# Kernel optimization log

Hardware: AMD Instinct MI355X
Metric: run time of the kernel (lower is better)

Reference implementation:

```python
import jax, jax.numpy as jnp
import numpy as np

N = 4096
IN_F = 512
OUT_F = 256
HEADS = 4
HEAD_DIM = OUT_F // HEADS


def setup_inputs() -> dict:
    key = jax.random.key(0)
    k_feat, k_adj, k_w, k_a = jax.random.split(key, 4)
    features = jax.random.normal(k_feat, (N, IN_F), dtype=jnp.float32)
    adj_matrix = jax.random.uniform(k_adj, (N, N), dtype=jnp.float32)
    # xavier-uniform-ish init scaled small
    W = jax.random.normal(k_w, (OUT_F, IN_F), dtype=jnp.float32) * (1.0 / np.sqrt(IN_F))
    a = jax.random.normal(k_a, (HEADS, 2 * HEAD_DIM), dtype=jnp.float32) * 0.1
    bias = jnp.zeros((OUT_F,), dtype=jnp.float32)
    return {"features": features, "adj_matrix": adj_matrix, "W": W, "a": a, "bias": bias}


def reference(features, adj_matrix, W, a, bias):
    n = features.shape[0]
    h = features @ W.T                      # [N, OUT_F]
    hh = h.reshape(n, HEADS, HEAD_DIM)      # [N, H, D]
    # e[i,j,h] = leaky_relu(<h_i, a[:, :D]> + <h_j, a[:, D:]>) -- additive decomposition
    e_src = jnp.einsum('nhd,hd->nh', hh, a[:, :HEAD_DIM])   # [N, H]
    e_dst = jnp.einsum('nhd,hd->nh', hh, a[:, HEAD_DIM:])   # [N, H]
    e = e_src[:, None, :] + e_dst[None, :, :]               # [N, N, H]
    e = jnp.where(e >= 0, e, 0.2 * e)                       # leaky_relu(0.2)
    mask = adj_matrix[:, :, None] > 0.1                     # [N, N, 1]
    e = jnp.where(mask, e, -jnp.inf)
    attention = jax.nn.softmax(e, axis=1)                   # softmax over j
    attention = jnp.nan_to_num(attention, nan=0.0)          # fully-masked rows -> 0
    attention_mean = attention.mean(axis=2)                 # [N, N]
    h_out = attention_mean @ h + bias                       # [N, OUT_F]
    return h_out
```

## Files before the change

### kernel.cpp

```cpp
#include <hip/hip_runtime.h>
#include <math.h>

#define NN      4096
#define INF_    512
#define OUTF    256
#define NHEAD   4
#define HDIM    64
#define KSPLIT  8

typedef __attribute__((ext_vector_type(8))) short  short8x;
typedef __attribute__((ext_vector_type(4))) float  float4x;
typedef __attribute__((ext_vector_type(2))) float  float2x;

__device__ __forceinline__ unsigned short f2bf(float x) {
    union { float f; unsigned int u; } c; c.f = x;
    unsigned int r = (c.u + 0x7FFFu + ((c.u >> 16) & 1u)) >> 16;
    return (unsigned short)r;
}
__device__ __forceinline__ unsigned int cvtpk_bf16(float lo, float hi) {
    unsigned int r;
    asm("v_cvt_pk_bf16_f32 %0, %1, %2" : "=v"(r) : "v"(lo), "v"(hi));
    return r;
}
__device__ __forceinline__ float2x bf2up(unsigned int u) {
    union { unsigned int x; float f; } lo, hi;
    lo.x = u << 16; hi.x = u & 0xFFFF0000u;
    float2x r; r[0] = lo.f; r[1] = hi.f; return r;
}
__device__ __forceinline__ float2x max2(float2x a, float2x b) {
    float2x r; r[0] = fmaxf(a[0], b[0]); r[1] = fmaxf(a[1], b[1]); return r;
}

__global__ __launch_bounds__(256) void k_cast(const float* __restrict__ feat,
                                              const float* __restrict__ W,
                                              const float* __restrict__ bias,
                                              unsigned short* __restrict__ featb,
                                              unsigned short* __restrict__ Wb,
                                              float* __restrict__ out) {
    const int b = blockIdx.x;
    const int tid = threadIdx.x;
    if (b >= 2176) {
        int idx = (b - 2176) * 1024 + tid * 4;
        float4x bv = *(const float4x*)(bias + ((tid * 4) & 255));
        *(float4x*)(out + idx) = bv;
        return;
    }
    const float* src;
    unsigned short* dst;
    int idx;
    if (b < 2048) { src = feat; dst = featb; idx = b * 1024 + tid * 4; }
    else          { src = W;    dst = Wb;    idx = (b - 2048) * 1024 + tid * 4; }
    float4x v = *(const float4x*)(src + idx);
    ushort4 u;
    u.x = f2bf(v[0]); u.y = f2bf(v[1]); u.z = f2bf(v[2]); u.w = f2bf(v[3]);
    *(ushort4*)(dst + idx) = u;
}

__global__ __launch_bounds__(256) void k_hedge(const unsigned short* __restrict__ featb,
                                               const unsigned short* __restrict__ Wb,
                                               const float* __restrict__ a,
                                               unsigned short* __restrict__ hT,
                                               float* __restrict__ es,
                                               unsigned short* __restrict__ Bt,
                                               unsigned short* __restrict__ Dt) {
    __shared__ __align__(16) unsigned short lds_f[32 * 40];
    __shared__ __align__(16) unsigned short lds_w[256 * 40];
    const int tid  = threadIdx.x;
    const int w    = tid >> 6;
    const int lane = tid & 63;
    const int lidx = lane & 15;
    const int quad = lane >> 4;
    const int i0   = blockIdx.x * 32;
    const int srf  = tid >> 3;
    const int skf  = (tid & 7) * 4;
    const int srw  = tid >> 2;
    const int skw  = (tid & 3) * 8;

    float4x acc[2][4];
    #pragma unroll
    for (int p = 0; p < 2; ++p)
        #pragma unroll
        for (int q = 0; q < 4; ++q)
            acc[p][q] = (float4x){0.f, 0.f, 0.f, 0.f};

    for (int kt = 0; kt < INF_; kt += 32) {
        __syncthreads();
        *(ushort4*)&lds_f[srf * 40 + skf] = *(const ushort4*)&featb[(size_t)(i0 + srf) * INF_ + kt + skf];
        #pragma unroll
        for (int itr = 0; itr < 4; ++itr) {
            int n = itr * 64 + srw;
            *(ushort4*)&lds_w[n * 40 + skw]     = *(const ushort4*)&Wb[(size_t)n * INF_ + kt + skw];
            *(ushort4*)&lds_w[n * 40 + skw + 4] = *(const ushort4*)&Wb[(size_t)n * INF_ + kt + skw + 4];
        }
        __syncthreads();
        short8x af[2], bw[4];
        #pragma unroll
        for (int t = 0; t < 2; ++t)
            af[t] = *(const short8x*)&lds_f[(t * 16 + lidx) * 40 + quad * 8];
        #pragma unroll
        for (int t = 0; t < 4; ++t)
            bw[t] = *(const short8x*)&lds_w[(w * 64 + t * 16 + lidx) * 40 + quad * 8];
        #pragma unroll
        for (int it = 0; it < 2; ++it)
            #pragma unroll
            for (int nt = 0; nt < 4; ++nt)
                acc[it][nt] = __builtin_amdgcn_mfma_f32_16x16x32_bf16(
                    af[it], bw[nt], acc[it][nt], 0, 0, 0);
    }
    #pragma unroll
    for (int it = 0; it < 2; ++it)
        #pragma unroll
        for (int nt = 0; nt < 4; ++nt) {
            int col = w * 64 + nt * 16 + lidx;
            int m0r = i0 + it * 16 + quad * 4;
            uint2 u;
            u.x = cvtpk_bf16(acc[it][nt][0], acc[it][nt][1]);
            u.y = cvtpk_bf16(acc[it][nt][2], acc[it][nt][3]);
            *(uint2*)&hT[(size_t)col * NN + m0r] = u;
        }
    float asrc[4], adst[4];
    #pragma unroll
    for (int nt = 0; nt < 4; ++nt) {
        asrc[nt] = a[w * 2 * HDIM + nt * 16 + lidx];
        adst[nt] = a[w * 2 * HDIM + HDIM + nt * 16 + lidx];
    }
    #pragma unroll
    for (int it = 0; it < 2; ++it)
        #pragma unroll
        for (int r = 0; r < 4; ++r) {
            float s = 0.f, d = 0.f;
            #pragma unroll
            for (int nt = 0; nt < 4; ++nt) {
                s += acc[it][nt][r] * asrc[nt];
                d += acc[it][nt][r] * adst[nt];
            }
            #pragma unroll
            for (int off = 1; off < 16; off <<= 1) {
                s += __shfl_xor(s, off);
                d += __shfl_xor(d, off);
            }
            if (lidx == 0) {
                int row = i0 + it * 16 + quad * 4 + r;
                es[row * NHEAD + w] = s;
                Bt[row * NHEAD + w] = f2bf(__expf(d));
                Dt[row * NHEAD + w] = f2bf(__expf(0.2f * d));
            }
        }
}

__global__ __launch_bounds__(256) void k_attn(const float* __restrict__ adj,
                                              const float* __restrict__ es,
                                              const unsigned short* __restrict__ Bt,
                                              const unsigned short* __restrict__ Dt,
                                              unsigned short* __restrict__ attn) {
    __shared__ float red[4][4];
    __shared__ float cfs[4];
    const int tid = threadIdx.x;
    const int wv  = tid >> 6;
    const int lane = tid & 63;
    const int i = blockIdx.x;

    const float4x esv = ((const float4x*)es)[i];
    float2x A01, A23, C01, C23;
    A01[0] = __expf(esv[0]); A01[1] = __expf(esv[1]);
    A23[0] = __expf(esv[2]); A23[1] = __expf(esv[3]);
    C01[0] = __expf(0.2f * esv[0]); C01[1] = __expf(0.2f * esv[1]);
    C23[0] = __expf(0.2f * esv[2]); C23[1] = __expf(0.2f * esv[3]);

    const float4x* arow4 = (const float4x*)(adj + (size_t)i * NN);
    const uint4* B4 = (const uint4*)Bt;
    const uint4* D4 = (const uint4*)Dt;

    float2x m01[4][4], m23[4][4];
    float2x den01 = (float2x){0.f, 0.f};
    float2x den23 = (float2x){0.f, 0.f};
    #pragma unroll
    for (int t = 0; t < 4; ++t) {
        int jv = t * 256 + tid;
        float4x av = arow4[jv];
        uint4 bu0 = B4[jv * 2], bu1 = B4[jv * 2 + 1];
        uint4 du0 = D4[jv * 2], du1 = D4[jv * 2 + 1];
        unsigned int bwv[8] = {bu0.x, bu0.y, bu0.z, bu0.w, bu1.x, bu1.y, bu1.z, bu1.w};
        unsigned int dwv[8] = {du0.x, du0.y, du0.z, du0.w, du1.x, du1.y, du1.z, du1.w};
        #pragma unroll
        for (int u = 0; u < 4; ++u) {
            float2x b01 = bf2up(bwv[u * 2]);
            float2x b23 = bf2up(bwv[u * 2 + 1]);
            float2x d01 = bf2up(dwv[u * 2]);
            float2x d23 = bf2up(dwv[u * 2 + 1]);
            float mf = (av[u] > 0.1f) ? 1.f : 0.f;
            float2x mf2; mf2[0] = mf; mf2[1] = mf;
            m01[t][u] = mf2 * max2(A01 * b01, C01 * d01);
            m23[t][u] = mf2 * max2(A23 * b23, C23 * d23);
            den01 += m01[t][u];
            den23 += m23[t][u];
        }
    }
    float dh[4] = {den01[0], den01[1], den23[0], den23[1]};
    #pragma unroll
    for (int off = 1; off < 64; off <<= 1) {
        #pragma unroll
        for (int h = 0; h < 4; ++h)
            dh[h] += __shfl_xor(dh[h], off);
    }
    if (lane == 0) {
        #pragma unroll
        for (int h = 0; h < 4; ++h) red[wv][h] = dh[h];
    }
    __syncthreads();
    if (tid < 4)
        cfs[tid] = red[0][tid] + red[1][tid] + red[2][tid] + red[3][tid];
    __syncthreads();
    float sc[4];
    #pragma unroll
    for (int h = 0; h < 4; ++h) {
        float den = cfs[h];
        sc[h] = den > 0.f ? 0.25f / den : 0.f;
    }

    unsigned short* orow = attn + (size_t)i * NN;
    #pragma unroll
    for (int t = 0; t < 4; ++t) {
        int jv = t * 256 + tid;
        float pv[4];
        #pragma unroll
        for (int u = 0; u < 4; ++u) {
            pv[u] = sc[0] * m01[t][u][0] + sc[1] * m01[t][u][1]
                  + sc[2] * m23[t][u][0] + sc[3] * m23[t][u][1];
        }
        uint2 o;
        o.x = cvtpk_bf16(pv[0], pv[1]);
        o.y = cvtpk_bf16(pv[2], pv[3]);
        *(uint2*)&orow[jv * 4] = o;
    }
}

__global__ __launch_bounds__(256) void k_out_gemm(const unsigned short* __restrict__ attn,
                                                  const unsigned short* __restrict__ hT,
                                                  float* __restrict__ out) {
    __shared__ __align__(16) unsigned short lds_a[32 * 40];
    __shared__ __align__(16) unsigned short lds_h[256 * 40];
    const int tid  = threadIdx.x;
    const int w    = tid >> 6;
    const int lane = tid & 63;
    const int lidx = lane & 15;
    const int quad = lane >> 4;
    const int i0    = blockIdx.x * 32;
    const int kbase = blockIdx.y * (NN / KSPLIT);
    const int srow = tid >> 3;
    const int skq  = tid & 7;

    float4x acc[2][4];
    #pragma unroll
    for (int p = 0; p < 2; ++p)
        #pragma unroll
        for (int q = 0; q < 4; ++q)
            acc[p][q] = (float4x){0.f, 0.f, 0.f, 0.f};

    ushort4 pa, ph[8];
    pa = *(const ushort4*)&attn[(size_t)(i0 + srow) * NN + kbase + skq * 4];
    #pragma unroll
    for (int it = 0; it < 8; ++it)
        ph[it] = *(const ushort4*)&hT[(size_t)(it * 32 + srow) * NN + kbase + skq * 4];

    const int KSTEPS = (NN / KSPLIT) / 32;
    for (int ks = 0; ks < KSTEPS; ++ks) {
        __syncthreads();
        *(ushort4*)&lds_a[srow * 40 + skq * 4] = pa;
        #pragma unroll
        for (int it = 0; it < 8; ++it)
            *(ushort4*)&lds_h[(it * 32 + srow) * 40 + skq * 4] = ph[it];
        __syncthreads();
        if (ks < KSTEPS - 1) {
            const int ktn = kbase + (ks + 1) * 32;
            pa = *(const ushort4*)&attn[(size_t)(i0 + srow) * NN + ktn + skq * 4];
            #pragma unroll
            for (int it = 0; it < 8; ++it)
                ph[it] = *(const ushort4*)&hT[(size_t)(it * 32 + srow) * NN + ktn + skq * 4];
        }
        short8x af[2], bfr[4];
        #pragma unroll
        for (int t = 0; t < 2; ++t)
            af[t]  = *(const short8x*)&lds_a[(t * 16 + lidx) * 40 + quad * 8];
        #pragma unroll
        for (int t = 0; t < 4; ++t)
            bfr[t] = *(const short8x*)&lds_h[(w * 64 + t * 16 + lidx) * 40 + quad * 8];
        #pragma unroll
        for (int it = 0; it < 2; ++it)
            #pragma unroll
            for (int nt = 0; nt < 4; ++nt)
                acc[it][nt] = __builtin_amdgcn_mfma_f32_16x16x32_bf16(
                    af[it], bfr[nt], acc[it][nt], 0, 0, 0);
    }
    #pragma unroll
    for (int it = 0; it < 2; ++it)
        #pragma unroll
        for (int nt = 0; nt < 4; ++nt)
            #pragma unroll
            for (int rr = 0; rr < 4; ++rr) {
                int row = i0 + it * 16 + quad * 4 + rr;
                int col = w * 64 + nt * 16 + lidx;
                unsafeAtomicAdd(&out[(size_t)row * OUTF + col], acc[it][nt][rr]);
            }
}

extern "C" void kernel_launch(void* const* d_in, const int* in_sizes, int n_in,
                              void* d_out, int out_size, void* d_ws, size_t ws_size,
                              hipStream_t stream) {
    const float* feat = (const float*)d_in[0];
    const float* adj  = (const float*)d_in[1];
    const float* W    = (const float*)d_in[2];
    const float* a    = (const float*)d_in[3];
    const float* bias = (const float*)d_in[4];
    float* out = (float*)d_out;

    char* ws = (char*)d_ws;
    float*          es    = (float*)(ws + 0);
    unsigned short* Btb   = (unsigned short*)(ws + (64u << 10));
    unsigned short* Dtb   = (unsigned short*)(ws + (96u << 10));
    unsigned short* hT    = (unsigned short*)(ws + (256u << 10));
    unsigned short* attn  = (unsigned short*)(ws + (2560u << 10));
    unsigned short* featb = (unsigned short*)(ws + (2560u << 10));
    unsigned short* Wb    = (unsigned short*)(ws + (6656u << 10));

    k_cast      <<<3200,              256, 0, stream>>>(feat, W, bias, featb, Wb, out);
    k_hedge     <<<128,               256, 0, stream>>>(featb, Wb, a, hT, es, Btb, Dtb);
    k_attn      <<<NN,                256, 0, stream>>>(adj, es, Btb, Dtb, attn);
    k_out_gemm  <<<dim3(128, KSPLIT), 256, 0, stream>>>(attn, hT, out);
}
```

Measured before the change: 178.6 us.

## Load MFMA fragments directly from global memory in output GEMM, drop LDS staging

New measurement: 212.6 us. +19.1%, slower.

```diff
diff --git a/kernel.cpp b/kernel.cpp
--- a/kernel.cpp
+++ b/kernel.cpp
@@ -6,7 +6,7 @@
 #define OUTF    256
 #define NHEAD   4
 #define HDIM    64
-#define KSPLIT  8
+#define KSPLIT  4
 
 typedef __attribute__((ext_vector_type(8))) short  short8x;
 typedef __attribute__((ext_vector_type(4))) float  float4x;
@@ -235,73 +235,66 @@
     }
 }
 
-__global__ __launch_bounds__(256) void k_out_gemm(const unsigned short* __restrict__ attn,
-                                                  const unsigned short* __restrict__ hT,
-                                                  float* __restrict__ out) {
-    __shared__ __align__(16) unsigned short lds_a[32 * 40];
-    __shared__ __align__(16) unsigned short lds_h[256 * 40];
+__global__ __launch_bounds__(256, 4) void k_out_gemm(const unsigned short* __restrict__ attn,
+                                                     const unsigned short* __restrict__ hT,
+                                                     float* __restrict__ out) {
     const int tid  = threadIdx.x;
     const int w    = tid >> 6;
     const int lane = tid & 63;
     const int lidx = lane & 15;
     const int quad = lane >> 4;
-    const int i0    = blockIdx.x * 32;
+    const int i0    = blockIdx.x * 16;
     const int kbase = blockIdx.y * (NN / KSPLIT);
-    const int srow = tid >> 3;
-    const int skq  = tid & 7;
-
-    float4x acc[2][4];
-    #pragma unroll
-    for (int p = 0; p < 2; ++p)
-        #pragma unroll
-        for (int q = 0; q < 4; ++q)
-            acc[p][q] = (float4x){0.f, 0.f, 0.f, 0.f};
-
-    ushort4 pa, ph[8];
-    pa = *(const ushort4*)&attn[(size_t)(i0 + srow) * NN + kbase + skq * 4];
-    #pragma unroll
-    for (int it = 0; it < 8; ++it)
-        ph[it] = *(const ushort4*)&hT[(size_t)(it * 32 + srow) * NN + kbase + skq * 4];
-
-    const int KSTEPS = (NN / KSPLIT) / 32;
-    for (int ks = 0; ks < KSTEPS; ++ks) {
-        __syncthreads();
-        *(ushort4*)&lds_a[srow * 40 + skq * 4] = pa;
-        #pragma unroll
-        for (int it = 0; it < 8; ++it)
-            *(ushort4*)&lds_h[(it * 32 + srow) * 40 + skq * 4] = ph[it];
-        __syncthreads();
-        if (ks < KSTEPS - 1) {
-            const int ktn = kbase + (ks + 1) * 32;
-            pa = *(const ushort4*)&attn[(size_t)(i0 + srow) * NN + ktn + skq * 4];
-            #pragma unroll
-            for (int it = 0; it < 8; ++it)
-                ph[it] = *(const ushort4*)&hT[(size_t)(it * 32 + srow) * NN + ktn + skq * 4];
-        }
-        short8x af[2], bfr[4];
-        #pragma unroll
-        for (int t = 0; t < 2; ++t)
-            af[t]  = *(const short8x*)&lds_a[(t * 16 + lidx) * 40 + quad * 8];
+
+    const unsigned short* arow = attn + (size_t)(i0 + lidx) * NN + kbase + quad * 8;
+    const unsigned short* hrow = hT   + (size_t)(w * 64 + lidx) * NN + kbase + quad * 8;
+
+    float4x acc[4];
+    #pragma unroll
+    for (int q = 0; q < 4; ++q)
+        acc[q] = (float4x){0.f, 0.f, 0.f, 0.f};
+
+    short8x ab[2][2];
+    short8x bb[2][8];
+
+    #pragma unroll
+    for (int hh = 0; hh < 2; ++hh) {
+        ab[0][hh] = *(const short8x*)(arow + hh * 32);
         #pragma unroll
         for (int t = 0; t < 4; ++t)
-            bfr[t] = *(const short8x*)&lds_h[(w * 64 + t * 16 + lidx) * 40 + quad * 8];
-        #pragma unroll
-        for (int it = 0; it < 2; ++it)
+            bb[0][t * 2 + hh] = *(const short8x*)(hrow + (size_t)t * 16 * NN + hh * 32);
+    }
+
+    const int NCHUNK = (NN / KSPLIT) / 64;
+    #pragma unroll
+    for (int it = 0; it < NCHUNK; ++it) {
+        const int cur = it & 1, nxt = cur ^ 1;
+        if (it + 1 < NCHUNK) {
+            const int ko = (it + 1) * 64;
+            #pragma unroll
+            for (int hh = 0; hh < 2; ++hh) {
+                ab[nxt][hh] = *(const short8x*)(arow + ko + hh * 32);
+                #pragma unroll
+                for (int t = 0; t < 4; ++t)
+                    bb[nxt][t * 2 + hh] = *(const short8x*)(hrow + (size_t)t * 16 * NN + ko + hh * 32);
+            }
+        }
+        #pragma unroll
+        for (int hh = 0; hh < 2; ++hh)
             #pragma unroll
             for (int nt = 0; nt < 4; ++nt)
-                acc[it][nt] = __builtin_amdgcn_mfma_f32_16x16x32_bf16(
-                    af[it], bfr[nt], acc[it][nt], 0, 0, 0);
-    }
-    #pragma unroll
-    for (int it = 0; it < 2; ++it)
-        #pragma unroll
-        for (int nt = 0; nt < 4; ++nt)
-            #pragma unroll
-            for (int rr = 0; rr < 4; ++rr) {
-                int row = i0 + it * 16 + quad * 4 + rr;
-                int col = w * 64 + nt * 16 + lidx;
-                unsafeAtomicAdd(&out[(size_t)row * OUTF + col], acc[it][nt][rr]);
-            }
+                acc[nt] = __builtin_amdgcn_mfma_f32_16x16x32_bf16(
+                    ab[cur][hh], bb[cur][nt * 2 + hh], acc[nt], 0, 0, 0);
+    }
+
+    #pragma unroll
+    for (int nt = 0; nt < 4; ++nt)
+        #pragma unroll
+        for (int rr = 0; rr < 4; ++rr) {
+            int row = i0 + quad * 4 + rr;
+            int col = w * 64 + nt * 16 + lidx;
+            unsafeAtomicAdd(&out[(size_t)row * OUTF + col], acc[nt][rr]);
+        }
 }
 
 extern "C" void kernel_launch(void* const* d_in, const int* in_sizes, int n_in,
@@ -326,5 +319,5 @@
     k_cast      <<<3200,              256, 0, stream>>>(feat, W, bias, featb, Wb, out);
     k_hedge     <<<128,               256, 0, stream>>>(featb, Wb, a, hT, es, Btb, Dtb);
     k_attn      <<<NN,                256, 0, stream>>>(adj, es, Btb, Dtb, attn);
-    k_out_gemm  <<<dim3(128, KSPLIT), 256, 0, stream>>>(attn, hT, out);
-}
+    k_out_gemm  <<<dim3(256, KSPLIT), 256, 0, stream>>>(attn, hT, out);
+}
```
